# Optimization experiments

Measured on AMD Instinct MI355X. Metric: run time of the kernel, lower is better.

The kernel has to match this reference:

```python
import jax, jax.numpy as jnp
import numpy as np

N, C, T, V, K = 32, 256, 64, 25, 3   # batch, in_channels, frames, joints, adjacency partitions
D = 256                               # out_channels
KT = 9                                # temporal kernel size
PAD = (KT - 1) // 2
EPS = 1e-5                            # BatchNorm eps (torch default)


def setup_inputs() -> dict:
    key = jax.random.key(0)
    ks = jax.random.split(key, 5)
    x = jax.random.normal(ks[0], (N, C, T, V), jnp.float32)
    A = jax.random.uniform(ks[1], (K, V, V), jnp.float32)           # learnable adjacency
    W_gcn = jax.random.normal(ks[2], (K, D, C), jnp.float32) * (2.0 / C) ** 0.5  # K stacked 1x1 convs
    b_gcn = jnp.zeros((K, D), jnp.float32)
    W_tcn = jax.random.normal(ks[3], (D, D, KT, 1), jnp.float32) * (2.0 / (D * KT)) ** 0.5  # kaiming fan_out
    b_tcn = jnp.zeros((D,), jnp.float32)
    gamma = jnp.ones((D,), jnp.float32)   # bn_init(bn, 1)
    beta = jnp.zeros((D,), jnp.float32)
    return dict(x=x, A=A, W_gcn=W_gcn, b_gcn=b_gcn, W_tcn=W_tcn,
                b_tcn=b_tcn, gamma=gamma, beta=beta)


def reference(x, A, W_gcn, b_gcn, W_tcn, b_tcn, gamma, beta):
    # ---- GCN: per-partition 1x1 conv over channels, then graph aggregation via A[k], summed over k ----
    # y[k,n,d,t,v] = sum_c W_gcn[k,d,c] * x[n,c,t,v] + b_gcn[k,d]
    y = jnp.einsum('kdc,nctv->kndtv', W_gcn, x) + b_gcn[:, None, :, None, None]
    # aggregate neighbors: sum_v y[k,n,d,t,v] * A[k,v,w], accumulated over partitions k
    y = jnp.einsum('kndtv,kvw->ndtw', y, A)        # [N, D, T, V]

    # ---- TCN: (9,1) temporal conv + BatchNorm2d (batch statistics) ----
    z = jax.lax.conv_general_dilated(
        y, W_tcn, window_strides=(1, 1), padding=((PAD, PAD), (0, 0)),
        dimension_numbers=('NCHW', 'OIHW', 'NCHW'))
    z = z + b_tcn[None, :, None, None]
    mean = jnp.mean(z, axis=(0, 2, 3), keepdims=True)
    var = jnp.mean((z - mean) ** 2, axis=(0, 2, 3), keepdims=True)  # biased, as torch BN training fwd
    z = gamma[None, :, None, None] * (z - mean) * jax.lax.rsqrt(var + EPS) + beta[None, :, None, None]

    # ---- residual (identity branch: in==out, stride==1) + ReLU ----
    return jax.nn.relu(z + x)
```

## Files before the change

kernel.cpp:

```cpp
#include <hip/hip_runtime.h>
#include <math.h>

typedef unsigned short u16;
typedef short v8s __attribute__((ext_vector_type(8)));
typedef float v4f __attribute__((ext_vector_type(4)));

#define AS1 __attribute__((address_space(1)))
#define AS3 __attribute__((address_space(3)))

__device__ __forceinline__ float bf2f(u16 u) {
    union { unsigned int i; float f; } c; c.i = ((unsigned int)u) << 16; return c.f;
}
__device__ __forceinline__ u16 f2bf(float f) {
    union { float f; unsigned int i; } c; c.f = f;
    unsigned int u = c.i;
    return (u16)((u + 0x7FFFu + ((u >> 16) & 1u)) >> 16);
}
__device__ __forceinline__ void gload_lds16(const void* g, void* l) {
    __builtin_amdgcn_global_load_lds((const AS1 void*)(uintptr_t)g,
                                     (AS3 void*)(unsigned int)(uintptr_t)l,
                                     16, 0, 0);
}

#define Nn 32
#define Tt 64
#define Vv 25
#define NP 51200
#define NBLK 200

__global__ __launch_bounds__(256) void prep_kernel(
    const float* __restrict__ Wg, const float* __restrict__ Wt,
    const float* __restrict__ A, const float* __restrict__ bg,
    u16* __restrict__ Wgb, u16* __restrict__ Wtb,
    float* __restrict__ bias2, float* __restrict__ zpad)
{
    const int idx = blockIdx.x * 256 + threadIdx.x;
    const int stride = gridDim.x * 256;
    for (int i = idx; i < 256 * 2304; i += stride) {
        int d = i / 2304, r = i - d * 2304, dt = r >> 8, c = r & 255;
        Wtb[i] = f2bf(Wt[(d * 256 + c) * 9 + dt]);
    }
    for (int i = idx; i < 256 * 768; i += stride) {
        int d = i / 768, r = i - d * 768, k = r >> 8, c = r & 255;
        Wgb[i] = f2bf(Wg[(k * 256 + d) * 256 + c]);
    }
    for (int i = idx; i < 25 * 256; i += stride) {
        int w = i >> 8, d = i & 255;
        float s = 0.f;
        for (int k = 0; k < 3; ++k) {
            float cs = 0.f;
            for (int v = 0; v < 25; ++v) cs += A[(k * 25 + v) * 25 + w];
            s += bg[k * 256 + d] * cs;
        }
        bias2[i] = s;
    }
    for (int i = idx; i < 256; i += stride) zpad[i] = 0.f;
}

__global__ __launch_bounds__(256) void xa_kernel(
    const float* __restrict__ x, const float* __restrict__ A,
    u16* __restrict__ xa2)
{
    const int t = blockIdx.x, n = blockIdx.y;
    const int tid = threadIdx.x;
    __shared__ float xs[256 * 25];

    for (int i = tid; i < 6400; i += 256) {
        int c = i / 25, v = i - c * 25;
        xs[i] = x[((n * 256 + c) * 64 + t) * 25 + v];
    }
    __syncthreads();

    float xr[25];
    #pragma unroll
    for (int v = 0; v < 25; ++v) xr[v] = xs[tid * 25 + v];

    const size_t pbase = ((size_t)n * 64 + t) * 25;
    #pragma unroll 1
    for (int k = 0; k < 3; ++k) {
        float o[25];
        #pragma unroll
        for (int w = 0; w < 25; ++w) {
            float acc = 0.f;
            #pragma unroll
            for (int v = 0; v < 25; ++v)
                acc = fmaf(xr[v], A[(k * 25 + v) * 25 + w], acc);
            o[w] = acc;
        }
        u16* dst = xa2 + k * 256 + tid;
        #pragma unroll
        for (int w = 0; w < 25; ++w)
            dst[(pbase + w) * 768] = f2bf(o[w]);
    }
}

template<int KTOT, bool TCN>
__global__ __launch_bounds__(512, 2) void gemm_kernel(
    const u16* __restrict__ Ad, const u16* __restrict__ Bw,
    const float* __restrict__ bias, u16* __restrict__ outB,
    float* __restrict__ psum, float* __restrict__ psq,
    const u16* __restrict__ zpad)
{
    constexpr int NT = KTOT / 64;
    __shared__ u16 smem[2][32768];

    const int tid = threadIdx.x;
    const int wid = tid >> 6, lane = tid & 63;
    const int lr = lane & 15, hk = lane >> 4;
    const int wm = wid >> 2, wn = wid & 3;
    const int rA = lane >> 3, sA = lane & 7;

    const int orig = blockIdx.x;
    const int m = (orig & 7) * 25 + (orig >> 3);

    v4f acc[8][4];
    const v4f vzero = {0.f, 0.f, 0.f, 0.f};
    #pragma unroll
    for (int mf = 0; mf < 8; ++mf)
        #pragma unroll
        for (int nf = 0; nf < 4; ++nf) acc[mf][nf] = vzero;

#define STAGE(buf, ktv)                                                        \
    {                                                                          \
        _Pragma("unroll")                                                      \
        for (int i = 0; i < 4; ++i) {                                          \
            const int ch = wid + i * 8;                             \
            const int row = ch * 8 + rA;                           \
            const int ss = sA ^ rA;                           \
            const u16* srcA;                                                   \
            if (TCN) {                                                         \
                const int dt = (ktv) >> 2, c0 = ((ktv)&3) << 6;                \
                const int p = m * 256 + row;                                   \
                const int t = (p % 1600) / 25;                                 \
                const int tp = t + dt - 4;                                     \
                srcA = ((unsigned)tp < 64u)                                    \
                     ? (Ad + (size_t)(p + (dt - 4) * 25) * 256 + c0 + ss * 8)  \
                     : zpad;                                                   \
            } else {                                                           \
                srcA = Ad + (size_t)(m * 256 + row) * 768 + (ktv)*64 + ss * 8; \
            }                                                                  \
            gload_lds16(srcA, (char*)&smem[buf][0] + ch * 1024);               \
            gload_lds16(Bw + (size_t)row * KTOT + (ktv)*64 + ss * 8,           \
                        (char*)&smem[buf][0] + 32768 + ch * 1024);             \
        }                                                                      \
    }

#define LDA_(dst, As_, mfv, kkv)                                               \
    {                                                                          \
        const int row = wm * 128 + (mfv)*16 + lr;                              \
        dst = *(const v8s*)((const char*)(As_) + row * 128 +                   \
                            ((((kkv)*4 + hk) ^ (row & 7)) << 4));              \
    }
#define LDB_(dst, Bs_, nfv, kkv)                                               \
    {                                                                          \
        const int row = wn * 64 + (nfv)*16 + lr;                               \
        dst = *(const v8s*)((const char*)(Bs_) + row * 128 +                   \
                            ((((kkv)*4 + hk) ^ (row & 7)) << 4));              \
    }

    STAGE(0, 0);
    if (NT > 1) STAGE(1, 1);
    if (NT > 1) asm volatile("s_waitcnt vmcnt(8)" ::: "memory");
    else        asm volatile("s_waitcnt vmcnt(0)" ::: "memory");
    __builtin_amdgcn_sched_barrier(0);
    __builtin_amdgcn_s_barrier();

    #pragma unroll 1
    for (int kt = 0; kt < NT; ++kt) {
        const int cur = kt & 1;
        const u16* As = &smem[cur][0];
        const u16* Bs = As + 16384;

        v8s a0[8], a1[8], b0[4], b1[4];
        #pragma unroll
        for (int nf = 0; nf < 4; ++nf) LDB_(b0[nf], Bs, nf, 0);
        #pragma unroll
        for (int mf = 0; mf < 8; ++mf) LDA_(a0[mf], As, mf, 0);
        #pragma unroll
        for (int nf = 0; nf < 4; ++nf) LDB_(b1[nf], Bs, nf, 1);
        #pragma unroll
        for (int mf = 0; mf < 8; ++mf) LDA_(a1[mf], As, mf, 1);
        asm volatile("s_waitcnt lgkmcnt(0)" ::: "memory");
        __builtin_amdgcn_sched_barrier(0);
        __builtin_amdgcn_s_barrier();
        __builtin_amdgcn_sched_barrier(0);

        if (kt + 2 < NT) STAGE(cur, kt + 2);
        __builtin_amdgcn_sched_barrier(0);

        __builtin_amdgcn_s_setprio(1);
        #pragma unroll
        for (int mf = 0; mf < 8; ++mf)
            #pragma unroll
            for (int nf = 0; nf < 4; ++nf)
                acc[mf][nf] = __builtin_amdgcn_mfma_f32_16x16x32_bf16(
                    a0[mf], b0[nf], acc[mf][nf], 0, 0, 0);
        #pragma unroll
        for (int mf = 0; mf < 8; ++mf)
            #pragma unroll
            for (int nf = 0; nf < 4; ++nf)
                acc[mf][nf] = __builtin_amdgcn_mfma_f32_16x16x32_bf16(
                    a1[mf], b1[nf], acc[mf][nf], 0, 0, 0);
        __builtin_amdgcn_s_setprio(0);
        __builtin_amdgcn_sched_barrier(0);

        if (kt + 2 < NT) {
            asm volatile("s_waitcnt vmcnt(8)" ::: "memory");
            __builtin_amdgcn_sched_barrier(0);
            __builtin_amdgcn_s_barrier();
        } else if (kt + 1 < NT) {
            asm volatile("s_waitcnt vmcnt(0)" ::: "memory");
            __builtin_amdgcn_sched_barrier(0);
            __builtin_amdgcn_s_barrier();
        }
    }
#undef STAGE
#undef LDA_
#undef LDB_

    if (!TCN) {
        #pragma unroll
        for (int mf = 0; mf < 8; ++mf) {
            #pragma unroll
            for (int j = 0; j < 4; ++j) {
                const int p = m * 256 + wm * 128 + mf * 16 + hk * 4 + j;
                const int w = p % 25;
                #pragma unroll
                for (int nf = 0; nf < 4; ++nf) {
                    const int d = wn * 64 + nf * 16 + lr;
                    outB[(size_t)p * 256 + d] = f2bf(acc[mf][nf][j] + bias[w * 256 + d]);
                }
            }
        }
    } else {
        float s[4], q[4];
        #pragma unroll
        for (int nf = 0; nf < 4; ++nf) {
            const int d = wn * 64 + nf * 16 + lr;
            const float bb = bias[d];
            s[nf] = 0.f; q[nf] = 0.f;
            #pragma unroll
            for (int mf = 0; mf < 8; ++mf) {
                #pragma unroll
                for (int j = 0; j < 4; ++j) {
                    const int p = m * 256 + wm * 128 + mf * 16 + hk * 4 + j;
                    const float zz = acc[mf][nf][j] + bb;
                    outB[(size_t)p * 256 + d] = f2bf(zz);
                    s[nf] += zz; q[nf] += zz * zz;
                }
            }
            s[nf] += __shfl_xor(s[nf], 16); s[nf] += __shfl_xor(s[nf], 32);
            q[nf] += __shfl_xor(q[nf], 16); q[nf] += __shfl_xor(q[nf], 32);
        }
        __syncthreads();
        float* red = (float*)&smem[0][0];
        if (hk == 0) {
            #pragma unroll
            for (int nf = 0; nf < 4; ++nf) {
                const int d = wn * 64 + nf * 16 + lr;
                red[wm * 256 + d] = s[nf];
                red[512 + wm * 256 + d] = q[nf];
            }
        }
        __syncthreads();
        if (tid < 256) {
            psum[(size_t)tid * NBLK + m] = red[tid] + red[256 + tid];
            psq[(size_t)tid * NBLK + m]  = red[512 + tid] + red[768 + tid];
        }
    }
}

__global__ __launch_bounds__(256) void bn_stats_kernel(
    const float* __restrict__ psum, const float* __restrict__ psq,
    const float* __restrict__ gamma, const float* __restrict__ beta,
    float* __restrict__ scale, float* __restrict__ shift)
{
    const int d = blockIdx.x, tid = threadIdx.x;
    float s = 0.f, q = 0.f;
    for (int i = tid; i < NBLK; i += 256) {
        s += psum[(size_t)d * NBLK + i];
        q += psq[(size_t)d * NBLK + i];
    }
    #pragma unroll
    for (int off = 32; off; off >>= 1) {
        s += __shfl_down(s, off);
        q += __shfl_down(q, off);
    }
    __shared__ float rs[4], rq[4];
    if ((tid & 63) == 0) { rs[tid >> 6] = s; rq[tid >> 6] = q; }
    __syncthreads();
    if (tid == 0) {
        s = rs[0] + rs[1] + rs[2] + rs[3];
        q = rq[0] + rq[1] + rq[2] + rq[3];
        const float mean = s / 51200.f;
        const float var = q / 51200.f - mean * mean;
        const float inv = rsqrtf(var + 1e-5f);
        scale[d] = gamma[d] * inv;
        shift[d] = beta[d] - gamma[d] * inv * mean;
    }
}

__global__ __launch_bounds__(256) void bn_apply_kernel(
    const u16* __restrict__ zb, const float* __restrict__ x,
    const float* __restrict__ scale, const float* __restrict__ shift,
    float* __restrict__ out)
{
    const int chunk = blockIdx.x;
    const int n = blockIdx.y;
    const int tid = threadIdx.x;
    __shared__ u16 zs[128 * 66];
    const size_t p0 = (size_t)n * 1600 + chunk * 64;

    for (int half = 0; half < 2; ++half) {
        const int d0 = half * 128;
        if (half) __syncthreads();
        for (int i = tid; i < 128 * 64; i += 256) {
            const int pl = i >> 7, dl = i & 127;
            zs[dl * 66 + pl] = zb[(p0 + pl) * 256 + d0 + dl];
        }
        __syncthreads();
        for (int i = tid; i < 128 * 64; i += 256) {
            const int dl = i >> 6, j = i & 63;
            const int d = d0 + dl;
            const size_t addr = ((size_t)n * 256 + d) * 1600 + chunk * 64 + j;
            const float r = bf2f(zs[dl * 66 + j]) * scale[d] + shift[d] + x[addr];
            out[addr] = fmaxf(r, 0.f);
        }
    }
}

extern "C" void kernel_launch(void* const* d_in, const int* in_sizes, int n_in,
                              void* d_out, int out_size, void* d_ws, size_t ws_size,
                              hipStream_t stream)
{
    const float* x     = (const float*)d_in[0];
    const float* A     = (const float*)d_in[1];
    const float* Wg    = (const float*)d_in[2];
    const float* bg    = (const float*)d_in[3];
    const float* Wt    = (const float*)d_in[4];
    const float* bt    = (const float*)d_in[5];
    const float* gamma = (const float*)d_in[6];
    const float* beta  = (const float*)d_in[7];
    float* out = (float*)d_out;

    char* w = (char*)d_ws;
    u16*   xa2   = (u16*)(w);
    u16*   y2T   = (u16*)(w + 78643200);
    u16*   zb    = (u16*)(w + 104857600);
    u16*   Wgb   = (u16*)(w + 131072000);
    u16*   Wtb   = (u16*)(w + 131465216);
    float* bias2 = (float*)(w + 132644864);
    float* psum  = (float*)(w + 132670464);
    float* psq   = (float*)(w + 133080064);
    float* scale = (float*)(w + 133489664);
    float* shift = (float*)(w + 133490688);
    float* zpad  = (float*)(w + 133491712);

    prep_kernel<<<128, 256, 0, stream>>>(Wg, Wt, A, bg, Wgb, Wtb, bias2, zpad);
    xa_kernel<<<dim3(64, 32), 256, 0, stream>>>(x, A, xa2);
    gemm_kernel<768, false><<<NBLK, 512, 0, stream>>>(xa2, Wgb, bias2, y2T,
                                                      nullptr, nullptr, (const u16*)zpad);
    gemm_kernel<2304, true><<<NBLK, 512, 0, stream>>>(y2T, Wtb, bt, zb,
                                                      psum, psq, (const u16*)zpad);
    bn_stats_kernel<<<256, 256, 0, stream>>>(psum, psq, gamma, beta, scale, shift);
    bn_apply_kernel<<<dim3(25, 32), 256, 0, stream>>>(zb, x, scale, shift, out);
}
```

Before: 186.3 us.

## Split GEMM k-step into four barrier-separated LDS-load/MFMA phases

Each k-tile iteration now loads half of the A fragments (four instead of eight) per half-k step and runs 16 MFMAs after each partial load, with a barrier and lgkmcnt wait in between. The global-to-LDS prefetch of tile kt+2 moves from before the MFMAs to after them. The aim is to cut fragment register pressure and interleave LDS reads with matrix math. In exchange it adds more workgroup barriers per iteration and gives less overlap between the global prefetch and compute. The barrier sits before the lgkmcnt wait, so LDS reads from other waves may still be in flight when the buffer is overwritten.

```diff
diff --git a/kernel.cpp b/kernel.cpp
--- a/kernel.cpp
+++ b/kernel.cpp
@@ -158,10 +158,28 @@
                             ((((kkv)*4 + hk) ^ (row & 7)) << 4));              \
     }
 
+#define LGK0_BAR_MFMA(AARR, BARR, MOFF)                                        \
+    __builtin_amdgcn_sched_barrier(0);                                         \
+    __builtin_amdgcn_s_barrier();                                              \
+    asm volatile("s_waitcnt lgkmcnt(0)" ::: "memory");                         \
+    __builtin_amdgcn_sched_barrier(0);                                         \
+    __builtin_amdgcn_s_setprio(1);                                             \
+    _Pragma("unroll")                                                          \
+    for (int mf = 0; mf < 4; ++mf)                                             \
+        _Pragma("unroll")                                                      \
+        for (int nf = 0; nf < 4; ++nf)                                         \
+            acc[(MOFF) + mf][nf] = __builtin_amdgcn_mfma_f32_16x16x32_bf16(    \
+                (AARR)[mf], (BARR)[nf], acc[(MOFF) + mf][nf], 0, 0, 0);        \
+    __builtin_amdgcn_s_setprio(0);                                             \
+    __builtin_amdgcn_sched_barrier(0);
+
     STAGE(0, 0);
-    if (NT > 1) STAGE(1, 1);
-    if (NT > 1) asm volatile("s_waitcnt vmcnt(8)" ::: "memory");
-    else        asm volatile("s_waitcnt vmcnt(0)" ::: "memory");
+    if (NT > 1) {
+        STAGE(1, 1);
+        asm volatile("s_waitcnt vmcnt(8)" ::: "memory");
+    } else {
+        asm volatile("s_waitcnt vmcnt(0)" ::: "memory");
+    }
     __builtin_amdgcn_sched_barrier(0);
     __builtin_amdgcn_s_barrier();
 
@@ -170,41 +188,30 @@
         const int cur = kt & 1;
         const u16* As = &smem[cur][0];
         const u16* Bs = As + 16384;
-
-        v8s a0[8], a1[8], b0[4], b1[4];
+        v8s b0[4], b1[4], aL[4], aH[4];
+
         #pragma unroll
         for (int nf = 0; nf < 4; ++nf) LDB_(b0[nf], Bs, nf, 0);
         #pragma unroll
-        for (int mf = 0; mf < 8; ++mf) LDA_(a0[mf], As, mf, 0);
+        for (int mf = 0; mf < 4; ++mf) LDA_(aL[mf], As, mf, 0);
+        LGK0_BAR_MFMA(aL, b0, 0)
+
+        #pragma unroll
+        for (int mf = 0; mf < 4; ++mf) LDA_(aH[mf], As, mf + 4, 0);
+        LGK0_BAR_MFMA(aH, b0, 4)
+
         #pragma unroll
         for (int nf = 0; nf < 4; ++nf) LDB_(b1[nf], Bs, nf, 1);
         #pragma unroll
-        for (int mf = 0; mf < 8; ++mf) LDA_(a1[mf], As, mf, 1);
-        asm volatile("s_waitcnt lgkmcnt(0)" ::: "memory");
-        __builtin_amdgcn_sched_barrier(0);
-        __builtin_amdgcn_s_barrier();
-        __builtin_amdgcn_sched_barrier(0);
-
-        if (kt + 2 < NT) STAGE(cur, kt + 2);
-        __builtin_amdgcn_sched_barrier(0);
-
-        __builtin_amdgcn_s_setprio(1);
-        #pragma unroll
-        for (int mf = 0; mf < 8; ++mf)
-            #pragma unroll
-            for (int nf = 0; nf < 4; ++nf)
-                acc[mf][nf] = __builtin_amdgcn_mfma_f32_16x16x32_bf16(
-                    a0[mf], b0[nf], acc[mf][nf], 0, 0, 0);
-        #pragma unroll
-        for (int mf = 0; mf < 8; ++mf)
-            #pragma unroll
-            for (int nf = 0; nf < 4; ++nf)
-                acc[mf][nf] = __builtin_amdgcn_mfma_f32_16x16x32_bf16(
-                    a1[mf], b1[nf], acc[mf][nf], 0, 0, 0);
-        __builtin_amdgcn_s_setprio(0);
-        __builtin_amdgcn_sched_barrier(0);
+        for (int mf = 0; mf < 4; ++mf) LDA_(aL[mf], As, mf, 1);
+        LGK0_BAR_MFMA(aL, b1, 0)
+
+        #pragma unroll
+        for (int mf = 0; mf < 4; ++mf) LDA_(aH[mf], As, mf + 4, 1);
+        LGK0_BAR_MFMA(aH, b1, 4)
 
         if (kt + 2 < NT) {
+            STAGE(cur, kt + 2);
             asm volatile("s_waitcnt vmcnt(8)" ::: "memory");
             __builtin_amdgcn_sched_barrier(0);
             __builtin_amdgcn_s_barrier();
@@ -217,6 +224,7 @@
 #undef STAGE
 #undef LDA_
 #undef LDB_
+#undef LGK0_BAR_MFMA
 
     if (!TCN) {
         #pragma unroll
```

Result: faster. 176.9 us, median of 2 (-5.0%).
